# Performance work log

Hardware: AMD Instinct MI355X
Metric: run time of the kernel (lower is better)

## Reference

```python
import jax, jax.numpy as jnp
import numpy as np

H = 2          # heads
C = 64         # hidden_dim per head
IN_DIM = 128
E_IN_DIM = 64
N_NODES = 50000
N_EDGES = 800000
NEG_SLOPE = 0.2


def gat_conv(x, edge_index, W, a_src, a_dst, bias):
    """PyG GATConv (heads=H, concat=False, add_self_loops=True).
    x: [N, F]; W: [F, H*C]; a_src/a_dst: [H, C]; bias: [C]."""
    N = x.shape[0]
    xw = (x @ W).reshape(N, H, C)                      # [N,H,C]
    loops = jnp.arange(N)
    src = jnp.concatenate([edge_index[0], loops])      # [E']
    dst = jnp.concatenate([edge_index[1], loops])
    a_s = jnp.einsum('nhc,hc->nh', xw, a_src)          # [N,H]
    a_d = jnp.einsum('nhc,hc->nh', xw, a_dst)
    e = jax.nn.leaky_relu(a_s[src] + a_d[dst], NEG_SLOPE)  # [E',H]
    # segment softmax over destination nodes (every node has a self-loop)
    m = jax.ops.segment_max(e, dst, num_segments=N)
    ex = jnp.exp(e - m[dst])
    den = jax.ops.segment_sum(ex, dst, num_segments=N)
    alpha = ex / den[dst]                              # [E',H]
    out = jax.ops.segment_sum(alpha[:, :, None] * xw[src], dst, num_segments=N)  # [N,H,C]
    return out.mean(axis=1) + bias                     # concat=False -> head mean


def setup_inputs() -> dict:
    key = jax.random.key(0)
    ks = jax.random.split(key, 16)
    s = 0.05
    return {
        'x': jax.random.normal(ks[0], (N_NODES, IN_DIM), jnp.float32),
        'xe': jax.random.normal(ks[1], (N_EDGES, E_IN_DIM), jnp.float32),
        'edge_index': jax.random.randint(ks[2], (2, N_EDGES), 0, N_NODES),
        # node GATConv params
        'Wn': jax.random.normal(ks[3], (IN_DIM, H * C), jnp.float32) * s,
        'asn': jax.random.normal(ks[4], (H, C), jnp.float32) * s,
        'adn': jax.random.normal(ks[5], (H, C), jnp.float32) * s,
        'bn': jnp.zeros((C,), jnp.float32),
        # edge GATConv params
        'We': jax.random.normal(ks[6], (E_IN_DIM, H * C), jnp.float32) * s,
        'ase': jax.random.normal(ks[7], (H, C), jnp.float32) * s,
        'ade': jax.random.normal(ks[8], (H, C), jnp.float32) * s,
        'be': jnp.zeros((C,), jnp.float32),
        # decoders
        'Wdx': jax.random.normal(ks[9], (C, IN_DIM), jnp.float32) * s,
        'bdx': jnp.zeros((IN_DIM,), jnp.float32),
        'Wde': jax.random.normal(ks[10], (C, E_IN_DIM), jnp.float32) * s,
        'bde': jnp.zeros((E_IN_DIM,), jnp.float32),
    }


def reference(x, xe, edge_index, Wn, asn, adn, bn, We, ase, ade, be, Wdx, bdx, Wde, bde):
    h_node = gat_conv(x, edge_index, Wn, asn, adn, bn)     # [N, C]
    h_edge = gat_conv(xe, edge_index, We, ase, ade, be)    # [E, C]
    x_rec = h_node @ Wdx + bdx                             # [N, in_dim]
    e_rec = h_edge @ Wde + bde                             # [E, edge_in_dim]
    return (x_rec, e_rec)
```

## Files before the change

### kernel.cpp

```cpp
#include <hip/hip_runtime.h>
#include <hip/hip_bf16.h>

constexpr int MAXD = 512;

__device__ __forceinline__ float lrelu(float v) { return v >= 0.f ? v : 0.2f * v; }

__global__ __launch_bounds__(256) void count_fold_kernel(
    const int* __restrict__ dst, int* __restrict__ cnt, int E, int nbCount,
    const float* __restrict__ We, const float* __restrict__ Wde,
    const float* __restrict__ be, const float* __restrict__ bde,
    float* __restrict__ M, float* __restrict__ b0) {
    int b = blockIdx.x;
    if (b < nbCount) {
        int e = b * 256 + threadIdx.x;
        if (e < E) atomicAdd(&cnt[dst[e]], 1);
    } else {
        int k = b - nbCount;
        int j = threadIdx.x;
        if (j >= 64) return;
        if (k < 64) {
            float s = 0.f;
            for (int c = 0; c < 64; c++)
                s = fmaf(0.5f * (We[k * 128 + c] + We[k * 128 + 64 + c]), Wde[c * 64 + j], s);
            M[k * 64 + j] = s;
        } else {
            float s = bde[j];
            for (int c = 0; c < 64; c++) s = fmaf(be[c], Wde[c * 64 + j], s);
            b0[j] = s;
        }
    }
}

__global__ __launch_bounds__(1024) void scan_kernel(const int* __restrict__ cnt, int* __restrict__ rowptr, int n) {
    __shared__ int part[1024];
    int t = threadIdx.x;
    int CH = (n + 1023) / 1024;
    int base = t * CH;
    int local = 0;
    for (int i = 0; i < CH; i++) { int idx = base + i; if (idx < n) local += cnt[idx]; }
    part[t] = local;
    __syncthreads();
    for (int o = 1; o < 1024; o <<= 1) {
        int v = (t >= o) ? part[t - o] : 0;
        __syncthreads();
        part[t] += v;
        __syncthreads();
    }
    int run = part[t] - local;
    for (int i = 0; i < CH; i++) {
        int idx = base + i;
        if (idx < n) { rowptr[idx] = run; run += cnt[idx]; }
    }
    if (t == 1023) rowptr[n] = run;
}

__global__ void scatter_kernel(const int* __restrict__ src, const int* __restrict__ dst,
                               int* __restrict__ cursor, int* __restrict__ ssrc, int E) {
    int e = blockIdx.x * blockDim.x + threadIdx.x;
    if (e < E) {
        int pos = atomicAdd(&cursor[dst[e]], 1);
        ssrc[pos] = src[e];
    }
}

template <int K>
__device__ __forceinline__ void enc_body(const float* __restrict__ X, const float* __restrict__ W,
                                         const float* __restrict__ avs, const float* __restrict__ avd,
                                         float* __restrict__ xw, float* __restrict__ a_s,
                                         float* __restrict__ a_d, int Nn, int bx, int h,
                                         float4* sA4, float4* sM4) {
    int tid = threadIdx.x;
    int tr = tid & 15;
    int tj = tid >> 4;
    int jc = h * 64;
    int tile0 = bx * 128;
    if (tile0 >= Nn) return;
    int nrows = min(128, Nn - tile0);

    float acc[8][4];
#pragma unroll
    for (int i = 0; i < 8; i++) { acc[i][0] = 0.f; acc[i][1] = 0.f; acc[i][2] = 0.f; acc[i][3] = 0.f; }

    for (int kc = 0; kc < K; kc += 64) {
        if (kc) __syncthreads();
#pragma unroll
        for (int it = 0; it < 4; it++) {
            int f = tid + it * 256;
            int k = f >> 4, jq = f & 15;
            sM4[f] = *(const float4*)(W + (size_t)(kc + k) * 128 + jc + 4 * jq);
        }
#pragma unroll
        for (int it = 0; it < 8; it++) {
            int e = tid + it * 256;
            int r = e >> 4, q = e & 15;
            int rs = (r < nrows) ? r : 0;
            sA4[(r << 4) | (q ^ (r & 15))] = *(const float4*)(X + (size_t)(tile0 + rs) * K + kc + 4 * q);
        }
        __syncthreads();
        for (int kq = 0; kq < 16; kq++) {
            float4 mf0 = sM4[(4 * kq + 0) * 16 + tj];
            float4 mf1 = sM4[(4 * kq + 1) * 16 + tj];
            float4 mf2 = sM4[(4 * kq + 2) * 16 + tj];
            float4 mf3 = sM4[(4 * kq + 3) * 16 + tj];
#pragma unroll
            for (int i = 0; i < 8; i++) {
                int row = tr + 16 * i;
                float4 af = sA4[(row << 4) | (kq ^ tr)];
                acc[i][0] = fmaf(af.x, mf0.x, acc[i][0]);
                acc[i][0] = fmaf(af.y, mf1.x, acc[i][0]);
                acc[i][0] = fmaf(af.z, mf2.x, acc[i][0]);
                acc[i][0] = fmaf(af.w, mf3.x, acc[i][0]);
                acc[i][1] = fmaf(af.x, mf0.y, acc[i][1]);
                acc[i][1] = fmaf(af.y, mf1.y, acc[i][1]);
                acc[i][1] = fmaf(af.z, mf2.y, acc[i][1]);
                acc[i][1] = fmaf(af.w, mf3.y, acc[i][1]);
                acc[i][2] = fmaf(af.x, mf0.z, acc[i][2]);
                acc[i][2] = fmaf(af.y, mf1.z, acc[i][2]);
                acc[i][2] = fmaf(af.z, mf2.z, acc[i][2]);
                acc[i][2] = fmaf(af.w, mf3.z, acc[i][2]);
                acc[i][3] = fmaf(af.x, mf0.w, acc[i][3]);
                acc[i][3] = fmaf(af.y, mf1.w, acc[i][3]);
                acc[i][3] = fmaf(af.z, mf2.w, acc[i][3]);
                acc[i][3] = fmaf(af.w, mf3.w, acc[i][3]);
            }
        }
    }

#pragma unroll
    for (int i = 0; i < 8; i++) {
        int row = tr + 16 * i;
        if (row < nrows) {
            float4 t = {acc[i][0], acc[i][1], acc[i][2], acc[i][3]};
            *(float4*)(xw + (size_t)(tile0 + row) * 128 + jc + 4 * tj) = t;
        }
    }

    float4 vs = *(const float4*)(avs + jc + 4 * tj);
    float4 vd = *(const float4*)(avd + jc + 4 * tj);
    __syncthreads();
    float* red = (float*)sA4;
#pragma unroll
    for (int i = 0; i < 8; i++) {
        int row = tr + 16 * i;
        float ps = acc[i][0] * vs.x + acc[i][1] * vs.y + acc[i][2] * vs.z + acc[i][3] * vs.w;
        float pd = acc[i][0] * vd.x + acc[i][1] * vd.y + acc[i][2] * vd.z + acc[i][3] * vd.w;
        red[row * 17 + tj] = ps;
        red[4096 + row * 17 + tj] = pd;
    }
    __syncthreads();
    if (tid < 128 && tid < nrows) {
        float ss = 0.f, sd = 0.f;
#pragma unroll
        for (int t = 0; t < 16; t++) { ss += red[tid * 17 + t]; sd += red[4096 + tid * 17 + t]; }
        a_s[(size_t)(tile0 + tid) * 2 + h] = ss;
        a_d[(size_t)(tile0 + tid) * 2 + h] = sd;
    }
}

__global__ __launch_bounds__(256) void enc_both(
    const float* __restrict__ x, const float* __restrict__ Wn, const float* __restrict__ asn,
    const float* __restrict__ adn, float* __restrict__ xw_n, float* __restrict__ a_sn, float* __restrict__ a_dn,
    const float* __restrict__ xe, const float* __restrict__ We, const float* __restrict__ ase,
    const float* __restrict__ ade, float* __restrict__ xw_e, float* __restrict__ a_se, float* __restrict__ a_de,
    int N) {
    __shared__ float4 sA4[128 * 16];
    __shared__ float4 sM4[64 * 16];
    if (blockIdx.z == 0)
        enc_body<128>(x, Wn, asn, adn, xw_n, a_sn, a_dn, N, blockIdx.x, blockIdx.y, sA4, sM4);
    else
        enc_body<64>(xe, We, ase, ade, xw_e, a_se, a_de, N, blockIdx.x, blockIdx.y, sA4, sM4);
}

template <int OD>
__device__ __forceinline__ void rowmap_body(const float* __restrict__ A, const float* __restrict__ M,
                                            const float* __restrict__ b0, float* __restrict__ out, int R,
                                            int bx, int by, float4* sA4, float4* sM4) {
    int tid = threadIdx.x;
    int tr = tid & 15;
    int tj = tid >> 4;
    int jc = by * 64;
    int tile0 = bx * 128;
    if (tile0 >= R) return;
    int nrows = min(128, R - tile0);

#pragma unroll
    for (int it = 0; it < 4; it++) {
        int f = tid + it * 256;
        int k = f >> 4, jq = f & 15;
        sM4[f] = *(const float4*)(M + (size_t)k * OD + jc + 4 * jq);
    }
    {
        const float4* Ag = (const float4*)(A + (size_t)tile0 * 64);
#pragma unroll
        for (int it = 0; it < 8; it++) {
            int e = tid + it * 256;
            int r = e >> 4, q = e & 15;
            int srcq = (r < nrows) ? e : q;
            sA4[(r << 4) | (q ^ (r & 15))] = Ag[srcq];
        }
    }
    __syncthreads();

    float4 b0v = *(const float4*)(b0 + jc + 4 * tj);
    float acc[8][4];
#pragma unroll
    for (int i = 0; i < 8; i++) { acc[i][0] = b0v.x; acc[i][1] = b0v.y; acc[i][2] = b0v.z; acc[i][3] = b0v.w; }

    for (int kq = 0; kq < 16; kq++) {
        float4 mf0 = sM4[(4 * kq + 0) * 16 + tj];
        float4 mf1 = sM4[(4 * kq + 1) * 16 + tj];
        float4 mf2 = sM4[(4 * kq + 2) * 16 + tj];
        float4 mf3 = sM4[(4 * kq + 3) * 16 + tj];
#pragma unroll
        for (int i = 0; i < 8; i++) {
            int row = tr + 16 * i;
            float4 af = sA4[(row << 4) | (kq ^ tr)];
            acc[i][0] = fmaf(af.x, mf0.x, acc[i][0]);
            acc[i][0] = fmaf(af.y, mf1.x, acc[i][0]);
            acc[i][0] = fmaf(af.z, mf2.x, acc[i][0]);
            acc[i][0] = fmaf(af.w, mf3.x, acc[i][0]);
            acc[i][1] = fmaf(af.x, mf0.y, acc[i][1]);
            acc[i][1] = fmaf(af.y, mf1.y, acc[i][1]);
            acc[i][1] = fmaf(af.z, mf2.y, acc[i][1]);
            acc[i][1] = fmaf(af.w, mf3.y, acc[i][1]);
            acc[i][2] = fmaf(af.x, mf0.z, acc[i][2]);
            acc[i][2] = fmaf(af.y, mf1.z, acc[i][2]);
            acc[i][2] = fmaf(af.z, mf2.z, acc[i][2]);
            acc[i][2] = fmaf(af.w, mf3.z, acc[i][2]);
            acc[i][3] = fmaf(af.x, mf0.w, acc[i][3]);
            acc[i][3] = fmaf(af.y, mf1.w, acc[i][3]);
            acc[i][3] = fmaf(af.z, mf2.w, acc[i][3]);
            acc[i][3] = fmaf(af.w, mf3.w, acc[i][3]);
        }
    }

#pragma unroll
    for (int i = 0; i < 8; i++) {
        int row = tr + 16 * i;
        if (row < nrows) {
            float4 t = {acc[i][0], acc[i][1], acc[i][2], acc[i][3]};
            *(float4*)(out + (size_t)(tile0 + row) * OD + jc + 4 * tj) = t;
        }
    }
}

__global__ __launch_bounds__(256) void rowmaps_all(
    const float* __restrict__ xeTail, const float* __restrict__ Mt, const float* __restrict__ b0t,
    float* __restrict__ outTail, int Rtail, int nbTail,
    const float* __restrict__ hm_n, const float* __restrict__ Wdx, const float* __restrict__ bdx,
    float* __restrict__ x_rec,
    const float* __restrict__ hm_e, const float* __restrict__ Wde, const float* __restrict__ bde,
    float* __restrict__ e_rec, int N, int nbDec) {
    __shared__ float4 sA4[128 * 16];
    __shared__ float4 sM4[64 * 16];
    int b = blockIdx.x;
    if (b < nbTail) {
        rowmap_body<64>(xeTail, Mt, b0t, outTail, Rtail, b, 0, sA4, sM4);
    } else if (b < nbTail + 2 * nbDec) {
        int bb = b - nbTail;
        rowmap_body<128>(hm_n, Wdx, bdx, x_rec, N, bb >> 1, bb & 1, sA4, sM4);
    } else {
        rowmap_body<64>(hm_e, Wde, bde, e_rec, N, b - nbTail - 2 * nbDec, 0, sA4, sM4);
    }
}

__global__ __launch_bounds__(128) void msg_fused(
    const float* __restrict__ xw_n, const float* __restrict__ a_sn, const float* __restrict__ a_dn,
    const float* __restrict__ xw_e, const float* __restrict__ a_se, const float* __restrict__ a_de,
    const int* __restrict__ rowptr, const int* __restrict__ ssrc,
    const float* __restrict__ bn, const float* __restrict__ be,
    float* __restrict__ hm_n, float* __restrict__ hm_e) {
    int n = blockIdx.x;
    int tid = threadIdx.x;
    int h = tid >> 6, c = tid & 63;
    __shared__ int s_src[MAXD];
    __shared__ float t_n[2][MAXD];
    __shared__ float t_e[2][MAXD];
    __shared__ float red[8];
    __shared__ float hsh[2][128];

    int base = rowptr[n];
    int deg = rowptr[n + 1] - base;
    int degc = min(deg, MAXD);

    float adn0 = a_dn[n * 2 + 0], adn1 = a_dn[n * 2 + 1];
    float ade0 = a_de[n * 2 + 0], ade1 = a_de[n * 2 + 1];
    float2 asn_n = *(const float2*)(a_sn + (size_t)n * 2);
    float2 ase_n = *(const float2*)(a_se + (size_t)n * 2);
    float es_n0 = lrelu(asn_n.x + adn0), es_n1 = lrelu(asn_n.y + adn1);
    float es_e0 = lrelu(ase_n.x + ade0), es_e1 = lrelu(ase_n.y + ade1);

    for (int i = tid; i < degc; i += 128) {
        int s = ssrc[base + i];
        s_src[i] = s;
        float2 an = *(const float2*)(a_sn + (size_t)s * 2);
        float2 ae = *(const float2*)(a_se + (size_t)s * 2);
        t_n[0][i] = lrelu(an.x + adn0);
        t_n[1][i] = lrelu(an.y + adn1);
        t_e[0][i] = lrelu(ae.x + ade0);
        t_e[1][i] = lrelu(ae.y + ade1);
    }
    __syncthreads();

    int w = tid >> 6;
    int lane = tid & 63;
    {
        const float(*tt)[MAXD] = w ? t_e : t_n;
        const float* asx = w ? a_se : a_sn;
        float ad0 = w ? ade0 : adn0, ad1 = w ? ade1 : adn1;
        float es0 = w ? es_e0 : es_n0, es1 = w ? es_e1 : es_n1;
        float m0 = es0, m1 = es1;
        for (int i = lane; i < degc; i += 64) { m0 = fmaxf(m0, tt[0][i]); m1 = fmaxf(m1, tt[1][i]); }
        for (int i = MAXD + lane; i < deg; i += 64) {
            int s = ssrc[base + i];
            float2 a = *(const float2*)(asx + (size_t)s * 2);
            m0 = fmaxf(m0, lrelu(a.x + ad0)); m1 = fmaxf(m1, lrelu(a.y + ad1));
        }
#pragma unroll
        for (int o = 1; o < 64; o <<= 1) { m0 = fmaxf(m0, __shfl_xor(m0, o)); m1 = fmaxf(m1, __shfl_xor(m1, o)); }
        float d0 = 0.f, d1 = 0.f;
        for (int i = lane; i < degc; i += 64) { d0 += __expf(tt[0][i] - m0); d1 += __expf(tt[1][i] - m1); }
        for (int i = MAXD + lane; i < deg; i += 64) {
            int s = ssrc[base + i];
            float2 a = *(const float2*)(asx + (size_t)s * 2);
            d0 += __expf(lrelu(a.x + ad0) - m0); d1 += __expf(lrelu(a.y + ad1) - m1);
        }
#pragma unroll
        for (int o = 1; o < 64; o <<= 1) { d0 += __shfl_xor(d0, o); d1 += __shfl_xor(d1, o); }
        d0 += __expf(es0 - m0);
        d1 += __expf(es1 - m1);
        if (lane == 0) { red[w * 4 + 0] = m0; red[w * 4 + 1] = m1; red[w * 4 + 2] = d0; red[w * 4 + 3] = d1; }
    }
    __syncthreads();

    for (int i = tid; i < degc; i += 128) {
        t_n[0][i] = __expf(t_n[0][i] - red[0]);
        t_n[1][i] = __expf(t_n[1][i] - red[1]);
        t_e[0][i] = __expf(t_e[0][i] - red[4]);
        t_e[1][i] = __expf(t_e[1][i] - red[5]);
    }
    __syncthreads();

    float mn = red[h], dn_ = red[2 + h];
    float me = red[4 + h], de_ = red[6 + h];
    float accn = __expf((h ? es_n1 : es_n0) - mn) * xw_n[(size_t)n * 128 + h * 64 + c];
    float acce = __expf((h ? es_e1 : es_e0) - me) * xw_e[(size_t)n * 128 + h * 64 + c];
    for (int i = 0; i < degc; i++) {
        int s = s_src[i];
        float wn_ = t_n[h][i];
        float we_ = t_e[h][i];
        accn = fmaf(wn_, xw_n[(size_t)s * 128 + h * 64 + c], accn);
        acce = fmaf(we_, xw_e[(size_t)s * 128 + h * 64 + c], acce);
    }
    for (int i = MAXD; i < deg; i++) {
        int s = ssrc[base + i];
        float2 an = *(const float2*)(a_sn + (size_t)s * 2);
        float2 ae = *(const float2*)(a_se + (size_t)s * 2);
        float tn_ = lrelu(h ? (an.y + adn1) : (an.x + adn0));
        float te_ = lrelu(h ? (ae.y + ade1) : (ae.x + ade0));
        accn = fmaf(__expf(tn_ - mn), xw_n[(size_t)s * 128 + h * 64 + c], accn);
        acce = fmaf(__expf(te_ - me), xw_e[(size_t)s * 128 + h * 64 + c], acce);
    }
    hsh[0][tid] = accn / dn_;
    hsh[1][tid] = acce / de_;
    __syncthreads();
    if (tid < 64) {
        hm_n[(size_t)n * 64 + tid] = fmaf(0.5f, hsh[0][tid] + hsh[0][64 + tid], bn[tid]);
        hm_e[(size_t)n * 64 + tid] = fmaf(0.5f, hsh[1][tid] + hsh[1][64 + tid], be[tid]);
    }
}

extern "C" void kernel_launch(void* const* d_in, const int* in_sizes, int n_in,
                              void* d_out, int out_size, void* d_ws, size_t ws_size,
                              hipStream_t stream) {
    const float* x   = (const float*)d_in[0];
    const float* xe  = (const float*)d_in[1];
    const int*   ei  = (const int*)d_in[2];
    const float* Wn  = (const float*)d_in[3];
    const float* asn = (const float*)d_in[4];
    const float* adn = (const float*)d_in[5];
    const float* bn  = (const float*)d_in[6];
    const float* We  = (const float*)d_in[7];
    const float* ase = (const float*)d_in[8];
    const float* ade = (const float*)d_in[9];
    const float* be  = (const float*)d_in[10];
    const float* Wdx = (const float*)d_in[11];
    const float* bdx = (const float*)d_in[12];
    const float* Wde = (const float*)d_in[13];
    const float* bde = (const float*)d_in[14];

    const int N  = in_sizes[0] / 128;
    const int NE = in_sizes[1] / 64;
    const int E  = in_sizes[2] / 2;
    const int* src = ei;
    const int* dst = ei + E;

    char* wsb = (char*)d_ws;
    size_t off = 0;
    auto alloc = [&](size_t bytes) -> void* {
        void* p = wsb + off;
        off += (bytes + 255) & ~(size_t)255;
        return p;
    };
    float* xw_n = (float*)alloc((size_t)N * 128 * 4);
    float* a_sn = (float*)alloc((size_t)N * 2 * 4);
    float* a_dn = (float*)alloc((size_t)N * 2 * 4);
    float* xw_e = (float*)alloc((size_t)N * 128 * 4);
    float* a_se = (float*)alloc((size_t)N * 2 * 4);
    float* a_de = (float*)alloc((size_t)N * 2 * 4);
    float* hm_n = (float*)alloc((size_t)N * 64 * 4);
    float* hm_e = (float*)alloc((size_t)N * 64 * 4);
    float* Mt   = (float*)alloc((size_t)64 * 64 * 4);
    float* b0t  = (float*)alloc((size_t)64 * 4);
    int* cnt    = (int*)alloc((size_t)(N + 1) * 4);
    int* rowptr = (int*)alloc((size_t)(N + 1) * 4);
    int* cursor = (int*)alloc((size_t)(N + 1) * 4);
    int* ssrc   = (int*)alloc((size_t)E * 4);

    float* x_rec = (float*)d_out;
    float* e_rec = (float*)d_out + (size_t)N * 128;

    hipMemsetAsync(cnt, 0, (size_t)N * 4, stream);
    int nbCount = (E + 255) / 256;
    count_fold_kernel<<<nbCount + 65, 256, 0, stream>>>(dst, cnt, E, nbCount, We, Wde, be, bde, Mt, b0t);
    scan_kernel<<<1, 1024, 0, stream>>>(cnt, rowptr, N);
    hipMemcpyAsync(cursor, rowptr, (size_t)N * 4, hipMemcpyDeviceToDevice, stream);
    scatter_kernel<<<(E + 255) / 256, 256, 0, stream>>>(src, dst, cursor, ssrc, E);

    enc_both<<<dim3((N + 127) / 128, 2, 2), 256, 0, stream>>>(
        x, Wn, asn, adn, xw_n, a_sn, a_dn,
        xe, We, ase, ade, xw_e, a_se, a_de, N);

    msg_fused<<<N, 128, 0, stream>>>(xw_n, a_sn, a_dn, xw_e, a_se, a_de, rowptr, ssrc, bn, be, hm_n, hm_e);

    {
        int Rtail = NE - N;
        int nbTail = (Rtail + 127) / 128;
        int nbDec = (N + 127) / 128;
        rowmaps_all<<<nbTail + 3 * nbDec, 256, 0, stream>>>(
            xe + (size_t)N * 64, Mt, b0t, e_rec + (size_t)N * 64, Rtail, nbTail,
            hm_n, Wdx, bdx, x_rec,
            hm_e, Wde, bde, e_rec, N, nbDec);
    }
}
```

Before: 750.4 us.

## Fold cursor init into scan and fuse scatter with encoder kernel

The scan kernel now writes the cursor array directly, which removes the device-to-device memcpy. The edge scatter and the node/edge encoder GEMMs are merged into a single launch, with block ranges dispatching to either role. This cuts two launches and lets the atomic-heavy scatter blocks run alongside the compute-bound encoder blocks. The trade-off is that the scatter blocks now carry the encoder's shared-memory footprint, which may lower their occupancy.

```diff
diff --git a/kernel.cpp b/kernel.cpp
--- a/kernel.cpp
+++ b/kernel.cpp
@@ -31,7 +31,8 @@
     }
 }
 
-__global__ __launch_bounds__(1024) void scan_kernel(const int* __restrict__ cnt, int* __restrict__ rowptr, int n) {
+__global__ __launch_bounds__(1024) void scan_kernel(const int* __restrict__ cnt, int* __restrict__ rowptr,
+                                                    int* __restrict__ cursor, int n) {
     __shared__ int part[1024];
     int t = threadIdx.x;
     int CH = (n + 1023) / 1024;
@@ -49,18 +50,9 @@
     int run = part[t] - local;
     for (int i = 0; i < CH; i++) {
         int idx = base + i;
-        if (idx < n) { rowptr[idx] = run; run += cnt[idx]; }
+        if (idx < n) { rowptr[idx] = run; cursor[idx] = run; run += cnt[idx]; }
     }
     if (t == 1023) rowptr[n] = run;
-}
-
-__global__ void scatter_kernel(const int* __restrict__ src, const int* __restrict__ dst,
-                               int* __restrict__ cursor, int* __restrict__ ssrc, int E) {
-    int e = blockIdx.x * blockDim.x + threadIdx.x;
-    if (e < E) {
-        int pos = atomicAdd(&cursor[dst[e]], 1);
-        ssrc[pos] = src[e];
-    }
 }
 
 template <int K>
@@ -157,7 +149,9 @@
     }
 }
 
-__global__ __launch_bounds__(256) void enc_both(
+__global__ __launch_bounds__(256) void scatter_enc(
+    const int* __restrict__ src, const int* __restrict__ dst,
+    int* __restrict__ cursor, int* __restrict__ ssrc, int E, int nbScatter, int gx,
     const float* __restrict__ x, const float* __restrict__ Wn, const float* __restrict__ asn,
     const float* __restrict__ adn, float* __restrict__ xw_n, float* __restrict__ a_sn, float* __restrict__ a_dn,
     const float* __restrict__ xe, const float* __restrict__ We, const float* __restrict__ ase,
@@ -165,10 +159,23 @@
     int N) {
     __shared__ float4 sA4[128 * 16];
     __shared__ float4 sM4[64 * 16];
-    if (blockIdx.z == 0)
-        enc_body<128>(x, Wn, asn, adn, xw_n, a_sn, a_dn, N, blockIdx.x, blockIdx.y, sA4, sM4);
-    else
-        enc_body<64>(xe, We, ase, ade, xw_e, a_se, a_de, N, blockIdx.x, blockIdx.y, sA4, sM4);
+    int b = blockIdx.x;
+    if (b < nbScatter) {
+        int e = b * 256 + threadIdx.x;
+        if (e < E) {
+            int pos = atomicAdd(&cursor[dst[e]], 1);
+            ssrc[pos] = src[e];
+        }
+    } else {
+        int idx = b - nbScatter;
+        int bx = idx % gx;
+        int rem = idx / gx;
+        int h = rem & 1, z = rem >> 1;
+        if (z == 0)
+            enc_body<128>(x, Wn, asn, adn, xw_n, a_sn, a_dn, N, bx, h, sA4, sM4);
+        else
+            enc_body<64>(xe, We, ase, ade, xw_e, a_se, a_de, N, bx, h, sA4, sM4);
+    }
 }
 
 template <int OD>
@@ -423,13 +430,16 @@
     hipMemsetAsync(cnt, 0, (size_t)N * 4, stream);
     int nbCount = (E + 255) / 256;
     count_fold_kernel<<<nbCount + 65, 256, 0, stream>>>(dst, cnt, E, nbCount, We, Wde, be, bde, Mt, b0t);
-    scan_kernel<<<1, 1024, 0, stream>>>(cnt, rowptr, N);
-    hipMemcpyAsync(cursor, rowptr, (size_t)N * 4, hipMemcpyDeviceToDevice, stream);
-    scatter_kernel<<<(E + 255) / 256, 256, 0, stream>>>(src, dst, cursor, ssrc, E);
-
-    enc_both<<<dim3((N + 127) / 128, 2, 2), 256, 0, stream>>>(
-        x, Wn, asn, adn, xw_n, a_sn, a_dn,
-        xe, We, ase, ade, xw_e, a_se, a_de, N);
+    scan_kernel<<<1, 1024, 0, stream>>>(cnt, rowptr, cursor, N);
+
+    {
+        int nbScatter = (E + 255) / 256;
+        int gx = (N + 127) / 128;
+        scatter_enc<<<nbScatter + 4 * gx, 256, 0, stream>>>(
+            src, dst, cursor, ssrc, E, nbScatter, gx,
+            x, Wn, asn, adn, xw_n, a_sn, a_dn,
+            xe, We, ase, ade, xw_e, a_se, a_de, N);
+    }
 
     msg_fused<<<N, 128, 0, stream>>>(xw_n, a_sn, a_dn, xw_e, a_se, a_de, rowptr, ssrc, bn, be, hm_n, hm_e);
 
```

Measured after the change: 796.1 us. 1.06x slower.
